# Kernel optimization log

Measured on AMD Instinct MI355X. Metric: run time of the kernel, lower is better.

The kernel has to match this reference:

```python
import jax, jax.numpy as jnp
import numpy as np

B, S, HID = 4, 4096, 1024
HEADS, D = 8, 128          # head_dim = HID // HEADS
NSEG, SEGLEN = 16, 256     # SEGLEN = S // NSEG
E, I = 16, 512             # num_experts, intermediate_size


def setup_inputs() -> dict:
    key = jax.random.key(0)
    ks = jax.random.split(key, 8)
    return {
        "x": jax.random.normal(ks[0], (B, S, HID), jnp.float32),
        "W_mh": jax.random.normal(ks[1], (HID, HID), jnp.float32) * (1.0 / np.sqrt(HID)),
        "b_mh": jax.random.normal(ks[2], (HID,), jnp.float32) * 0.02,
        "W_merge": jax.random.normal(ks[3], (HID, HID), jnp.float32) * (1.0 / np.sqrt(HID)),
        "b_merge": jnp.zeros((HID,), jnp.float32),
        "expert_embeddings": jax.random.normal(ks[4], (D, E), jnp.float32) * (1.0 / np.sqrt(D)),
        "first_linear": jax.random.normal(ks[5], (E, I, D), jnp.float32) * (1.0 / np.sqrt(D)),
        "second_linear": jax.random.normal(ks[6], (E, D, I), jnp.float32) * (1.0 / np.sqrt(I)),
    }


def reference(x, W_mh, b_mh, W_merge, b_merge, expert_embeddings, first_linear, second_linear):
    # multi-head projection
    x = x @ W_mh.T + b_mh                                   # [B,S,HID]
    # split into segments/heads (faithful to torch reshape order)
    x = x.reshape(B, NSEG, SEGLEN, HEADS, D)                # [B,N,L,H,D]
    avg = jnp.mean(x, axis=2)                               # [B,N,H,D]
    # router: softmax over experts
    ew = jax.nn.softmax(jnp.einsum('bnhd,de->bnhe', avg, expert_embeddings), axis=-1)
    # merge expert weight matrices (equivalent to torch's broadcast-mul-sum)
    m1 = jnp.einsum('eid,bnhe->bnhid', first_linear, ew)    # [B,N,H,I,D]
    m2 = jnp.einsum('edi,bnhe->bnhdi', second_linear, ew)   # [B,N,H,D,I]
    # NOTE: torch uses reshape (not permute) here -> mixes seglen/head axes; replicate.
    xr = x.reshape(B, NSEG, HEADS, SEGLEN, D)               # [B,N,H,L,D]
    # causal shift: segment s uses weights from segment s-1
    x_causal = xr[:, 1:]
    h = jax.nn.relu(jnp.einsum('bnhld,bnhid->bnhli', x_causal, m1[:, :-1]))
    res = jnp.einsum('bnhli,bnhdi->bnhld', h, m2[:, :-1])   # [B,N-1,H,L,D]
    # segment 0 special case (no_grad in torch -> stop_gradient)
    h0 = jax.nn.relu(jnp.einsum('bhld,bhid->bhli', xr[:, 0], m1[:, 0]))
    r0 = jnp.einsum('bhli,bhdi->bhld', h0, m2[:, 0])
    r0 = jax.lax.stop_gradient(r0)[:, None]                 # [B,1,H,L,D]
    out = jnp.concatenate([r0, res], axis=1)                # [B,N,H,L,D]
    out = out.reshape(B, S, HEADS, D).reshape(B, S, HID)
    return out @ W_merge.T + b_merge
```

## Files before the change

kernel.cpp:

```cpp
#include <hip/hip_runtime.h>
#include <hip/hip_bf16.h>

typedef _Float16 f16;
typedef f16 f16x2 __attribute__((ext_vector_type(2)));
typedef f16 f16x4 __attribute__((ext_vector_type(4)));
typedef f16 f16x8 __attribute__((ext_vector_type(8)));
typedef float f32x2 __attribute__((ext_vector_type(2)));
typedef float f32x4 __attribute__((ext_vector_type(4)));

#define MFMA16(a, b, c) __builtin_amdgcn_mfma_f32_16x16x32_f16(a, b, c, 0, 0, 0)

__device__ __forceinline__ void glds16(const void* g, void* l) {
    __builtin_amdgcn_global_load_lds(
        (const __attribute__((address_space(1))) unsigned int*)g,
        (__attribute__((address_space(3))) unsigned int*)l, 16, 0, 0);
}

__global__ __launch_bounds__(256) void cvt_kernel(const float* __restrict__ s,
                                                  f16* __restrict__ d, int n) {
    int i = (blockIdx.x * 256 + threadIdx.x) * 8;
    if (i >= n) return;
    float4 a = *(const float4*)(s + i);
    float4 b = *(const float4*)(s + i + 4);
    f16x8 h;
    h[0] = (f16)a.x; h[1] = (f16)a.y; h[2] = (f16)a.z; h[3] = (f16)a.w;
    h[4] = (f16)b.x; h[5] = (f16)b.y; h[6] = (f16)b.z; h[7] = (f16)b.w;
    *(f16x8*)(d + i) = h;
}


template <int MH, int NH, bool LOADA>
__device__ __forceinline__ void phase_rw(const f16* Aslab, const f16* Bslab,
                                         f16x8 (&af)[4][2], f16x8 (&bf)[2][2],
                                         int cl, int q, int wm, int wn) {
    if (LOADA) {
#pragma unroll
        for (int mt = 0; mt < 4; ++mt)
#pragma unroll
            for (int ks = 0; ks < 2; ++ks)
                af[mt][ks] =
                    *(const f16x8*)&Aslab[(wm * 64 + mt * 16 + cl) * 64 +
                                          ((ks * 4 + q) ^ (cl & 7)) * 8];
    }
#pragma unroll
    for (int nt = 0; nt < 2; ++nt)
#pragma unroll
        for (int ks = 0; ks < 2; ++ks)
            bf[nt][ks] = *(const f16x8*)&Bslab[(wn * 32 + nt * 16 + cl) * 64 +
                                               ((ks * 4 + q) ^ (cl & 7)) * 8];
}

template <int MH, int NH>
__device__ __forceinline__ void phase_mm(f16x8 (&af)[4][2], f16x8 (&bf)[2][2],
                                         f32x4 (&acc)[8][4]) {
    __builtin_amdgcn_s_setprio(1);
#pragma unroll
    for (int mt = 0; mt < 4; ++mt)
#pragma unroll
        for (int nt = 0; nt < 2; ++nt)
#pragma unroll
            for (int ks = 0; ks < 2; ++ks)
                acc[MH * 4 + mt][NH * 2 + nt] =
                    MFMA16(af[mt][ks], bf[nt][ks], acc[MH * 4 + mt][NH * 2 + nt]);
    __builtin_amdgcn_s_setprio(0);
}

__device__ __forceinline__ void stage_half(const f16* gsrc, int ldk, f16* ldst,
                                           int w, int lane) {
#pragma unroll
    for (int j = 0; j < 2; ++j) {
        int idx = j * 512 + w * 64 + lane;
        int rr = idx >> 3;
        int gs = (idx & 7) ^ (rr & 7);
        glds16(gsrc + (size_t)rr * ldk + gs * 8, ldst + (j * 512 + w * 64) * 8);
    }
}

#define VM8 asm volatile("s_waitcnt vmcnt(8)" ::: "memory")
#define VM6 asm volatile("s_waitcnt vmcnt(6)" ::: "memory")
#define VM4 asm volatile("s_waitcnt vmcnt(4)" ::: "memory")
#define VM0 asm volatile("s_waitcnt vmcnt(0)" ::: "memory")
#define VMN do {} while (0)
#define SB0 __builtin_amdgcn_sched_barrier(0)

#define SA(DB, H, KT) stage_half(A16 + (size_t)(mb * 256 + (H)*128) * K + (KT)*64, \
                                 K, Ad[DB][H], w, lane)
#define SBm(DB, H, KT) stage_half(Bw + (size_t)(nb * 256 + (H)*128) * K + (KT)*64, \
                                  K, Bd[DB][H], w, lane)

#define PH(DB, MH, NH, LA, STAGE, VMC)                                    \
    phase_rw<MH, NH, LA>(Ad[DB][MH], Bd[DB][NH], af, bf, cl, q, wm, wn);  \
    STAGE;                                                                \
    SB0; __builtin_amdgcn_s_barrier(); SB0;                               \
    phase_mm<MH, NH>(af, bf, acc);                                        \
    VMC;                                                                  \
    SB0; __builtin_amdgcn_s_barrier(); SB0;

template <bool OUT_F16>
__global__ __launch_bounds__(512, 2) void gemm256_kernel(
    const f16* __restrict__ A16, const f16* __restrict__ Bw,
    const float* __restrict__ bias, void* __restrict__ C_, int M, int N, int K) {
    __shared__ f16 Ad[2][2][128 * 64];
    __shared__ f16 Bd[2][2][128 * 64];
    const int tid = threadIdx.x;
    const int lane = tid & 63;
    const int w = tid >> 6;
    const int wm = w >> 2, wn = w & 3;
    const int q = lane >> 4, cl = lane & 15;
    const int nblk = N >> 8;
    const int cpx = (int)gridDim.x >> 3;
    const int logical = ((int)blockIdx.x & 7) * cpx + ((int)blockIdx.x >> 3);
    const int mb = logical / nblk, nb = logical % nblk;

    f32x4 acc[8][4] = {};
    f16x8 af[4][2], bf[2][2];
    const int ITERS = (K >> 6) / 2;

    SA(0, 0, 0); SBm(0, 0, 0); SBm(0, 1, 0); SA(0, 1, 0);
    SA(1, 0, 1); SBm(1, 0, 1);
    VM8;
    SB0; __builtin_amdgcn_s_barrier(); SB0;

#pragma unroll 1
    for (int i = 0; i < ITERS - 1; ++i) {
        const int k2 = 2 * i;
        PH(0, 0, 0, true,  SA(1, 1, k2 + 1),  VM8)
        PH(0, 0, 1, false, SBm(1, 1, k2 + 1), VM8)
        PH(0, 1, 0, true,  SA(0, 0, k2 + 2),  VMN)
        PH(0, 1, 1, false, SBm(0, 0, k2 + 2), VM8)
        PH(1, 0, 0, true,  SBm(0, 1, k2 + 2), VM6)
        PH(1, 0, 1, false, SA(0, 1, k2 + 2),  VMN)
        PH(1, 1, 0, true,  SA(1, 0, k2 + 3),  VMN)
        PH(1, 1, 1, false, SBm(1, 0, k2 + 3), VM8)
    }
    {
        const int kl = 2 * ITERS - 1;
        PH(0, 0, 0, true,  SA(1, 1, kl),  VM8)
        PH(0, 0, 1, false, SBm(1, 1, kl), VM8)
        PH(0, 1, 0, true,  VMN,           VMN)
        PH(0, 1, 1, false, VMN,           VM4)
        PH(1, 0, 0, true,  VMN,           VM0)
        PH(1, 0, 1, false, VMN,           VMN)
        PH(1, 1, 0, true,  VMN,           VMN)
        PH(1, 1, 1, false, VMN,           VMN)
    }

#pragma unroll
    for (int mt7 = 0; mt7 < 8; ++mt7) {
#pragma unroll
        for (int nt4 = 0; nt4 < 4; ++nt4) {
            int row0 = mb * 256 + (mt7 >> 2) * 128 + wm * 64 + (mt7 & 3) * 16 + q * 4;
            int col = nb * 256 + (nt4 >> 1) * 128 + wn * 32 + (nt4 & 1) * 16 + cl;
            float bv = bias[col];
#pragma unroll
            for (int r = 0; r < 4; ++r) {
                float v = acc[mt7][nt4][r] + bv;
                if (OUT_F16)
                    ((f16*)C_)[(size_t)(row0 + r) * N + col] = (f16)v;
                else
                    ((float*)C_)[(size_t)(row0 + r) * N + col] = v;
            }
        }
    }
}

__global__ __launch_bounds__(256) void avg_kernel(const f16* __restrict__ X1h,
                                                  float* __restrict__ partial) {
    const int bn = blockIdx.x >> 2, rc = blockIdx.x & 3;
    const int tid = threadIdx.x;
    const f16* base = X1h + (size_t)bn * 262144 + (size_t)rc * 65536 + tid * 4;
    float s0 = 0.f, s1 = 0.f, s2 = 0.f, s3 = 0.f;
    for (int l = 0; l < 64; ++l) {
        f16x4 v = *(const f16x4*)(base + (size_t)l * 1024);
        s0 += (float)v[0]; s1 += (float)v[1]; s2 += (float)v[2]; s3 += (float)v[3];
    }
    const float sc = 1.f / 256.f;
    float4 o = make_float4(s0 * sc, s1 * sc, s2 * sc, s3 * sc);
    *(float4*)(partial + (size_t)(bn * 4 + rc) * 1024 + tid * 4) = o;
}

__global__ __launch_bounds__(64) void router_kernel(const float* __restrict__ partial,
                                                    const float* __restrict__ emb,
                                                    float* __restrict__ ew) {
    const int t = blockIdx.x;
    const int bn = t >> 3, h = t & 7;
    const int lane = threadIdx.x;
    float acc = 0.f;
    const float* p = partial + (size_t)bn * 4096 + h * 128;
    if (lane < 16) {
        for (int d = 0; d < 128; ++d) {
            float a = p[d] + p[d + 1024] + p[d + 2048] + p[d + 3072];
            acc = fmaf(a, emb[d * 16 + lane], acc);
        }
    }
    float m = acc;
#pragma unroll
    for (int o = 8; o; o >>= 1) m = fmaxf(m, __shfl_xor(m, o));
    float pr = __expf(acc - m);
    float s = pr;
#pragma unroll
    for (int o = 8; o; o >>= 1) s += __shfl_xor(s, o);
    if (lane < 16) ew[t * 16 + lane] = pr / s;
}

__global__ __launch_bounds__(256) void mix_kernel(const float* __restrict__ ew,
                                                  const float* __restrict__ FL,
                                                  const float* __restrict__ SL,
                                                  f16* __restrict__ m1h,
                                                  f16* __restrict__ m2h) {
    const int bid = blockIdx.x;
    const int which = bid >> 10;
    const int tg = (bid >> 6) & 15;
    const int chunk = bid & 63;
    const float* src = which ? SL : FL;
    f16* dst = which ? m2h : m1h;
    const int tid = threadIdx.x;
    const int e0 = chunk * 1024 + tid * 4;

    f32x4 fl[16];
#pragma unroll
    for (int e = 0; e < 16; ++e)
        fl[e] = *(const f32x4*)(src + (size_t)e * 65536 + e0);

    const float* wbase = ew + (size_t)tg * 32 * 16;
    float wc[16];
#pragma unroll
    for (int e = 0; e < 16; ++e) wc[e] = wbase[e];

#pragma unroll 1
    for (int tt = 0; tt < 32; ++tt) {
        float wn2[16];
        if (tt < 31) {
#pragma unroll
            for (int e = 0; e < 16; ++e) wn2[e] = wbase[(tt + 1) * 16 + e];
        }
        f32x4 a = {0.f, 0.f, 0.f, 0.f};
#pragma unroll
        for (int e = 0; e < 16; ++e) {
            a[0] = fmaf(wc[e], fl[e][0], a[0]);
            a[1] = fmaf(wc[e], fl[e][1], a[1]);
            a[2] = fmaf(wc[e], fl[e][2], a[2]);
            a[3] = fmaf(wc[e], fl[e][3], a[3]);
        }
        f16x4 h;
        h[0] = (f16)a[0]; h[1] = (f16)a[1]; h[2] = (f16)a[2]; h[3] = (f16)a[3];
        *(f16x4*)(dst + (size_t)(tg * 32 + tt) * 65536 + e0) = h;
        if (tt < 31) {
#pragma unroll
            for (int e = 0; e < 16; ++e) wc[e] = wn2[e];
        }
    }
}

__device__ __forceinline__ void stage_w128(const f16* __restrict__ src, f16* lds,
                                           int w, int lane, int rowstride) {
#pragma unroll
    for (int it = 0; it < 8; ++it) {
        int cbase = it * 256 + w * 64;
        int c = cbase + lane;
        int row = c >> 4, pc = c & 15;
        int lc = pc ^ (row & 7);
        glds16(src + (size_t)row * rowstride + lc * 8, lds + cbase * 8);
    }
}

__global__ __launch_bounds__(256) void mlp_kernel(const f16* __restrict__ Xg,
                                                  const f16* __restrict__ m1h,
                                                  const f16* __restrict__ m2h,
                                                  f16* __restrict__ Yg) {
    __shared__ f16 Hs[128 * 128];
    __shared__ f16 Ws[128 * 128];
    const int cpx = (int)gridDim.x >> 3;
    const int logical = ((int)blockIdx.x & 7) * cpx + ((int)blockIdx.x >> 3);
    const int t = logical >> 1, lh = logical & 1;
    const int n = (t >> 3) & 15;
    const int tm = (n > 0) ? (t - 8) : t;
    const int tid = threadIdx.x;
    const int lane = tid & 63, w = tid >> 6;
    const int q = lane >> 4, cl = lane & 15;
    const int l0 = w * 32;

    const f16* Xsrc = Xg + (size_t)t * 32768 + lh * 16384;
    const f16* m1b = m1h + (size_t)tm * 65536;
    const f16* m2b = m2h + (size_t)tm * 65536;

    f16x8 xf[2][4];
#pragma unroll
    for (int lt = 0; lt < 2; ++lt) {
        int l = l0 + lt * 16 + cl;
#pragma unroll
        for (int ks = 0; ks < 4; ++ks)
            xf[lt][ks] = *(const f16x8*)(Xsrc + (size_t)l * 128 + ks * 32 + q * 8);
    }
    stage_w128(m1b, Ws, w, lane, 128);
    __syncthreads();

    f32x4 acc2[2][8] = {};
#pragma unroll 1
    for (int ic = 0; ic < 4; ++ic) {
#pragma unroll
        for (int it = 0; it < 8; ++it) {
            f16x8 af2[4];
#pragma unroll
            for (int ks = 0; ks < 4; ++ks) {
                int r = it * 16 + cl;
                int ch = (ks * 4 + q) ^ (r & 7);
                af2[ks] = *(const f16x8*)&Ws[r * 128 + ch * 8];
            }
            f32x4 a1[2] = {};
#pragma unroll
            for (int ks = 0; ks < 4; ++ks)
#pragma unroll
                for (int lt = 0; lt < 2; ++lt)
                    a1[lt] = MFMA16(af2[ks], xf[lt][ks], a1[lt]);
            int ibase = it * 16 + q * 4;
            int ch = ibase >> 3;
            int sub = (q & 1) * 8;
#pragma unroll
            for (int lt = 0; lt < 2; ++lt) {
                int l = l0 + lt * 16 + cl;
                f16x4 hv;
                hv[0] = (f16)fmaxf(a1[lt][0], 0.f);
                hv[1] = (f16)fmaxf(a1[lt][1], 0.f);
                hv[2] = (f16)fmaxf(a1[lt][2], 0.f);
                hv[3] = (f16)fmaxf(a1[lt][3], 0.f);
                *(f16x4*)((char*)Hs + (size_t)l * 256 + ((ch ^ (l & 7)) << 4) + sub) = hv;
            }
        }
        __syncthreads();
        stage_w128(m2b + ic * 128, Ws, w, lane, 512);
        __syncthreads();

        f16x8 hf[2][4];
#pragma unroll
        for (int lt = 0; lt < 2; ++lt) {
            int l = l0 + lt * 16 + cl;
#pragma unroll
            for (int ks = 0; ks < 4; ++ks) {
                int ch = (ks * 4 + q) ^ (l & 7);
                hf[lt][ks] = *(const f16x8*)&Hs[l * 128 + ch * 8];
            }
        }
#pragma unroll
        for (int nt = 0; nt < 8; ++nt) {
            f16x8 bf2[4];
#pragma unroll
            for (int ks = 0; ks < 4; ++ks) {
                int r = nt * 16 + cl;
                int ch = (ks * 4 + q) ^ (r & 7);
                bf2[ks] = *(const f16x8*)&Ws[r * 128 + ch * 8];
            }
#pragma unroll
            for (int lt = 0; lt < 2; ++lt)
#pragma unroll
                for (int ks = 0; ks < 4; ++ks)
                    acc2[lt][nt] = MFMA16(hf[lt][ks], bf2[ks], acc2[lt][nt]);
        }
        __syncthreads();
        if (ic < 3) {
            stage_w128(m1b + (size_t)(ic + 1) * 16384, Ws, w, lane, 128);
            __syncthreads();
        }
    }
    f16* Yb = Yg + (size_t)t * 32768 + lh * 16384;
#pragma unroll
    for (int lt = 0; lt < 2; ++lt) {
#pragma unroll
        for (int nt = 0; nt < 8; ++nt) {
            int lr = l0 + lt * 16 + q * 4;
            int d = nt * 16 + cl;
#pragma unroll
            for (int r = 0; r < 4; ++r)
                Yb[(size_t)(lr + r) * 128 + d] = (f16)acc2[lt][nt][r];
        }
    }
}

extern "C" void kernel_launch(void* const* d_in, const int* in_sizes, int n_in,
                              void* d_out, int out_size, void* d_ws, size_t ws_size,
                              hipStream_t stream) {
    const float* x    = (const float*)d_in[0];
    const float* W_mh = (const float*)d_in[1];
    const float* b_mh = (const float*)d_in[2];
    const float* W_mg = (const float*)d_in[3];
    const float* b_mg = (const float*)d_in[4];
    const float* emb  = (const float*)d_in[5];
    const float* FL   = (const float*)d_in[6];
    const float* SL   = (const float*)d_in[7];

    char* ws = (char*)d_ws;
    f16*   X1h  = (f16*)(ws + 0);
    f16*   m1h  = (f16*)(ws + 33554432);
    f16*   X0h  = (f16*)(ws + 33554432);
    f16*   m2h  = (f16*)(ws + 100663296);
    f16*   Wmhh = (f16*)(ws + 167772160);
    f16*   Wmgh = (f16*)(ws + 169869312);
    float* part = (float*)(ws + 171966464);
    float* ew   = (float*)(ws + 173015040);

    cvt_kernel<<<512, 256, 0, stream>>>(W_mh, Wmhh, 1048576);
    cvt_kernel<<<512, 256, 0, stream>>>(W_mg, Wmgh, 1048576);
    cvt_kernel<<<8192, 256, 0, stream>>>(x, X0h, 16777216);
    gemm256_kernel<true><<<256, 512, 0, stream>>>(X0h, Wmhh, b_mh, X1h,
                                                  16384, 1024, 1024);
    avg_kernel<<<256, 256, 0, stream>>>(X1h, part);
    router_kernel<<<512, 64, 0, stream>>>(part, emb, ew);
    mix_kernel<<<2048, 256, 0, stream>>>(ew, FL, SL, m1h, m2h);
    mlp_kernel<<<1024, 256, 0, stream>>>(X1h, m1h, m2h, X1h);
    gemm256_kernel<false><<<256, 512, 0, stream>>>(X1h, Wmgh, b_mg, d_out,
                                                   16384, 1024, 1024);
}
```

Before: 209.5 us.

## Double-buffer expert weight chunks in MLP kernel to overlap loads with MFMA

```diff
diff --git a/kernel.cpp b/kernel.cpp
--- a/kernel.cpp
+++ b/kernel.cpp
@@ -15,6 +15,13 @@
         (const __attribute__((address_space(1))) unsigned int*)g,
         (__attribute__((address_space(3))) unsigned int*)l, 16, 0, 0);
 }
+
+#define VM8 asm volatile("s_waitcnt vmcnt(8)" ::: "memory")
+#define VM6 asm volatile("s_waitcnt vmcnt(6)" ::: "memory")
+#define VM4 asm volatile("s_waitcnt vmcnt(4)" ::: "memory")
+#define VM0 asm volatile("s_waitcnt vmcnt(0)" ::: "memory")
+#define VMN do {} while (0)
+#define SB0 __builtin_amdgcn_sched_barrier(0)
 
 __global__ __launch_bounds__(256) void cvt_kernel(const float* __restrict__ s,
                                                   f16* __restrict__ d, int n) {
@@ -28,7 +35,6 @@
     *(f16x8*)(d + i) = h;
 }
 
-
 template <int MH, int NH, bool LOADA>
 __device__ __forceinline__ void phase_rw(const f16* Aslab, const f16* Bslab,
                                          f16x8 (&af)[4][2], f16x8 (&bf)[2][2],
@@ -75,13 +81,6 @@
         glds16(gsrc + (size_t)rr * ldk + gs * 8, ldst + (j * 512 + w * 64) * 8);
     }
 }
-
-#define VM8 asm volatile("s_waitcnt vmcnt(8)" ::: "memory")
-#define VM6 asm volatile("s_waitcnt vmcnt(6)" ::: "memory")
-#define VM4 asm volatile("s_waitcnt vmcnt(4)" ::: "memory")
-#define VM0 asm volatile("s_waitcnt vmcnt(0)" ::: "memory")
-#define VMN do {} while (0)
-#define SB0 __builtin_amdgcn_sched_barrier(0)
 
 #define SA(DB, H, KT) stage_half(A16 + (size_t)(mb * 256 + (H)*128) * K + (KT)*64, \
                                  K, Ad[DB][H], w, lane)
@@ -252,15 +251,22 @@
     }
 }
 
-__device__ __forceinline__ void stage_w128(const f16* __restrict__ src, f16* lds,
-                                           int w, int lane, int rowstride) {
-#pragma unroll
-    for (int it = 0; it < 8; ++it) {
-        int cbase = it * 256 + w * 64;
-        int c = cbase + lane;
-        int row = c >> 4, pc = c & 15;
-        int lc = pc ^ (row & 7);
-        glds16(src + (size_t)row * rowstride + lc * 8, lds + cbase * 8);
+__device__ __forceinline__ void stage_m1(const f16* m1c, f16* dst, int w, int lane) {
+#pragma unroll
+    for (int j = 0; j < 4; ++j) {
+        int idx = j * 256 + w * 64 + lane;
+        int row = idx >> 4, g = idx & 15;
+        glds16(m1c + (size_t)row * 128 + (g ^ (row & 7)) * 8,
+               dst + (j * 256 + w * 64) * 8);
+    }
+}
+__device__ __forceinline__ void stage_m2(const f16* m2c, f16* dst, int w, int lane) {
+#pragma unroll
+    for (int j = 0; j < 4; ++j) {
+        int idx = j * 256 + w * 64 + lane;
+        int row = idx >> 3, g = idx & 7;
+        glds16(m2c + (size_t)row * 512 + (g ^ (row & 7)) * 8,
+               dst + (j * 256 + w * 64) * 8);
     }
 }
 
@@ -268,8 +274,9 @@
                                                   const f16* __restrict__ m1h,
                                                   const f16* __restrict__ m2h,
                                                   f16* __restrict__ Yg) {
-    __shared__ f16 Hs[128 * 128];
-    __shared__ f16 Ws[128 * 128];
+    __shared__ f16 W1[2][64 * 128];
+    __shared__ f16 W2[2][128 * 64];
+    __shared__ f16 Hs[128 * 64];
     const int cpx = (int)gridDim.x >> 3;
     const int logical = ((int)blockIdx.x & 7) * cpx + ((int)blockIdx.x >> 3);
     const int t = logical >> 1, lh = logical & 1;
@@ -284,6 +291,8 @@
     const f16* m1b = m1h + (size_t)tm * 65536;
     const f16* m2b = m2h + (size_t)tm * 65536;
 
+    stage_m1(m1b, W1[0], w, lane);
+    stage_m2(m2b, W2[0], w, lane);
     f16x8 xf[2][4];
 #pragma unroll
     for (int lt = 0; lt < 2; ++lt) {
@@ -292,20 +301,24 @@
         for (int ks = 0; ks < 4; ++ks)
             xf[lt][ks] = *(const f16x8*)(Xsrc + (size_t)l * 128 + ks * 32 + q * 8);
     }
-    stage_w128(m1b, Ws, w, lane, 128);
-    __syncthreads();
+    VM0;
+    SB0; __builtin_amdgcn_s_barrier(); SB0;
 
     f32x4 acc2[2][8] = {};
 #pragma unroll 1
-    for (int ic = 0; ic < 4; ++ic) {
-#pragma unroll
-        for (int it = 0; it < 8; ++it) {
+    for (int ic = 0; ic < 8; ++ic) {
+        const int pb = ic & 1, ob = pb ^ 1;
+        if (ic < 7) stage_m1(m1b + (size_t)(ic + 1) * 8192, W1[ob], w, lane);
+        SB0;
+        __builtin_amdgcn_s_setprio(1);
+#pragma unroll
+        for (int it = 0; it < 4; ++it) {
             f16x8 af2[4];
 #pragma unroll
             for (int ks = 0; ks < 4; ++ks) {
                 int r = it * 16 + cl;
-                int ch = (ks * 4 + q) ^ (r & 7);
-                af2[ks] = *(const f16x8*)&Ws[r * 128 + ch * 8];
+                af2[ks] = *(const f16x8*)&W1[pb][r * 128 +
+                                                (((ks * 4 + q) ^ (r & 7))) * 8];
             }
             f32x4 a1[2] = {};
 #pragma unroll
@@ -313,8 +326,7 @@
 #pragma unroll
                 for (int lt = 0; lt < 2; ++lt)
                     a1[lt] = MFMA16(af2[ks], xf[lt][ks], a1[lt]);
-            int ibase = it * 16 + q * 4;
-            int ch = ibase >> 3;
+            int gi = 2 * it + (q >> 1);
             int sub = (q & 1) * 8;
 #pragma unroll
             for (int lt = 0; lt < 2; ++lt) {
@@ -324,44 +336,46 @@
                 hv[1] = (f16)fmaxf(a1[lt][1], 0.f);
                 hv[2] = (f16)fmaxf(a1[lt][2], 0.f);
                 hv[3] = (f16)fmaxf(a1[lt][3], 0.f);
-                *(f16x4*)((char*)Hs + (size_t)l * 256 + ((ch ^ (l & 7)) << 4) + sub) = hv;
+                *(f16x4*)((char*)Hs + (size_t)l * 128 + ((gi ^ (l & 7)) << 4) + sub) =
+                    hv;
             }
         }
-        __syncthreads();
-        stage_w128(m2b + ic * 128, Ws, w, lane, 512);
-        __syncthreads();
-
-        f16x8 hf[2][4];
-#pragma unroll
-        for (int lt = 0; lt < 2; ++lt) {
-            int l = l0 + lt * 16 + cl;
-#pragma unroll
-            for (int ks = 0; ks < 4; ++ks) {
-                int ch = (ks * 4 + q) ^ (l & 7);
-                hf[lt][ks] = *(const f16x8*)&Hs[l * 128 + ch * 8];
+        __builtin_amdgcn_s_setprio(0);
+        if (ic < 7) { VM4; } else { VM0; }
+        SB0; __builtin_amdgcn_s_barrier(); SB0;
+
+        if (ic < 7) stage_m2(m2b + (ic + 1) * 64, W2[ob], w, lane);
+        SB0;
+        f16x8 hf[2][2];
+#pragma unroll
+        for (int lt = 0; lt < 2; ++lt)
+#pragma unroll
+            for (int ks = 0; ks < 2; ++ks) {
+                int l = l0 + lt * 16 + cl;
+                hf[lt][ks] =
+                    *(const f16x8*)&Hs[l * 64 + (((ks * 4 + q) ^ (l & 7))) * 8];
             }
-        }
+        __builtin_amdgcn_s_setprio(1);
 #pragma unroll
         for (int nt = 0; nt < 8; ++nt) {
-            f16x8 bf2[4];
-#pragma unroll
-            for (int ks = 0; ks < 4; ++ks) {
-                int r = nt * 16 + cl;
-                int ch = (ks * 4 + q) ^ (r & 7);
-                bf2[ks] = *(const f16x8*)&Ws[r * 128 + ch * 8];
+            f16x8 bf2[2];
+#pragma unroll
+            for (int ks = 0; ks < 2; ++ks) {
+                int d = nt * 16 + cl;
+                bf2[ks] = *(const f16x8*)&W2[pb][d * 64 +
+                                                 (((ks * 4 + q) ^ (d & 7))) * 8];
             }
 #pragma unroll
             for (int lt = 0; lt < 2; ++lt)
 #pragma unroll
-                for (int ks = 0; ks < 4; ++ks)
+                for (int ks = 0; ks < 2; ++ks)
                     acc2[lt][nt] = MFMA16(hf[lt][ks], bf2[ks], acc2[lt][nt]);
         }
-        __syncthreads();
-        if (ic < 3) {
-            stage_w128(m1b + (size_t)(ic + 1) * 16384, Ws, w, lane, 128);
-            __syncthreads();
-        }
-    }
+        __builtin_amdgcn_s_setprio(0);
+        if (ic < 7) { VM4; }
+        SB0; __builtin_amdgcn_s_barrier(); SB0;
+    }
+
     f16* Yb = Yg + (size_t)t * 32768 + lh * 16384;
 #pragma unroll
     for (int lt = 0; lt < 2; ++lt) {
```

Result: no change. 210.7 us (+0.6%).
